# Kernel optimization log

Measured on AMD Instinct MI355X. Metric: run time of the kernel, lower is better.

The kernel has to match this reference:

```python
import jax, jax.numpy as jnp
import numpy as np

NUM_TAGS = 128
BATCH = 128
SEQ = 1024


def setup_inputs() -> dict:
    key = jax.random.key(0)
    k1, k2, k3, k4, k5 = jax.random.split(key, 5)
    emissions = jax.random.normal(k1, (BATCH, SEQ, NUM_TAGS), dtype=jnp.float32)
    tags = jax.random.randint(k2, (BATCH, SEQ), 0, NUM_TAGS, dtype=jnp.int32)
    mask = jnp.ones((BATCH, SEQ), dtype=bool)
    transitions = jax.random.normal(k3, (NUM_TAGS, NUM_TAGS), dtype=jnp.float32)
    start_transitions = jax.random.normal(k4, (NUM_TAGS,), dtype=jnp.float32)
    end_transitions = jax.random.normal(k5, (NUM_TAGS,), dtype=jnp.float32)
    return {
        "emissions": emissions,
        "tags": tags,
        "mask": mask,
        "transitions": transitions,
        "start_transitions": start_transitions,
        "end_transitions": end_transitions,
    }


def _forward_score(emissions, transitions, start_t, end_t, tags, mask):
    # score of the gold path; fully vectorized over time
    first = start_t[tags[:, 0]] + jnp.take_along_axis(emissions[:, 0], tags[:, 0:1], axis=1)[:, 0]
    trans = transitions[tags[:, :-1], tags[:, 1:]]                         # [B, S-1]
    emit = jnp.take_along_axis(emissions[:, 1:], tags[:, 1:, None], axis=2)[..., 0]  # [B, S-1]
    m = mask[:, 1:].astype(emissions.dtype)
    score = first + jnp.sum((trans + emit) * m, axis=1)
    last_idx = jnp.sum(mask, axis=1).astype(jnp.int32) - 1                 # [B]
    last_tags = jnp.take_along_axis(tags, last_idx[:, None], axis=1)[:, 0]
    return score + end_t[last_tags]


def _partition(emissions, transitions, start_t, end_t, mask):
    # log-partition via forward algorithm, single persistent scan over time
    alpha0 = start_t + emissions[:, 0]                                     # [B, T]

    def step(alpha, xs):
        e, mk = xs                                                         # e: [B,T], mk: [B] bool
        # alpha[b,i] + transitions[i,j] + e[b,j]  -> logsumexp over i
        nxt = jax.nn.logsumexp(alpha[:, :, None] + transitions[None, :, :] + e[:, None, :], axis=1)
        return jnp.where(mk[:, None], nxt, alpha), None

    em_t = jnp.swapaxes(emissions[:, 1:], 0, 1)                            # [S-1, B, T]
    mk_t = jnp.swapaxes(mask[:, 1:], 0, 1)                                 # [S-1, B]
    alpha, _ = jax.lax.scan(step, alpha0, (em_t, mk_t))
    return jax.nn.logsumexp(alpha + end_t, axis=1)                         # [B]


def reference(emissions, tags, mask, transitions, start_transitions, end_transitions):
    logZ = _partition(emissions, transitions, start_transitions, end_transitions, mask)
    gold = _forward_score(emissions, transitions, start_transitions, end_transitions, tags, mask)
    return jnp.mean(logZ - gold)
```

## Files before the change

kernel.cpp:

```cpp
#include <hip/hip_runtime.h>

#define NT 128
#define BATCH 128
#define SEQ 1024
#define NSCAN 256

__device__ __forceinline__ float wave_sum64(float x) {
  float y = x;
  asm volatile(
    "v_add_f32 %0, %0, %0 row_shr:1 bound_ctrl:0\n\t"
    "v_add_f32 %0, %0, %0 row_shr:2 bound_ctrl:0\n\t"
    "v_add_f32 %0, %0, %0 row_shr:4 bound_ctrl:0\n\t"
    "v_add_f32 %0, %0, %0 row_shr:8 bound_ctrl:0\n\t"
    "v_add_f32 %0, %0, %0 row_bcast:15 row_mask:0xa\n\t"
    "v_add_f32 %0, %0, %0 row_bcast:31 row_mask:0xc\n\t"
    : "+v"(y));
  return __uint_as_float(__builtin_amdgcn_readlane(__float_as_uint(y), 63));
}

__global__ __attribute__((amdgpu_waves_per_eu(2, 4))) __launch_bounds__(512)
void crf_fused(const float* __restrict__ em, const int* __restrict__ tags,
               const float* __restrict__ trans,
               const float* __restrict__ start_t,
               const float* __restrict__ end_t,
               float* __restrict__ state_out,
               float* __restrict__ shift_out,
               float* __restrict__ gold)
{
  __shared__ float PART[2][4][NT];
  __shared__ float SUMS[2][4];
  __shared__ int   tg[SEQ];
  __shared__ float red[8];

  const int tid = threadIdx.x;
  const int bid = blockIdx.x;

  if (bid < NSCAN) {
    const int l = tid & 63;
    const int w = tid >> 6;
    const int h = w >> 2;
    const int q = w & 3;
    const int b = bid & (BATCH - 1);
    const bool fwd = (bid < BATCH);
    const int jout = h * 64 + l;
    const int isl  = q * 32 + (l & 31);
    const float* emb = em + (size_t)b * SEQ * NT;

    float E[32];
#pragma unroll
    for (int k = 0; k < 32; ++k) {
      float t = fwd ? trans[(q * 32 + k) * NT + jout]
                    : trans[jout * NT + q * 32 + k];
      E[k] = __expf(t);
    }

    const int nsteps = fwd ? 512 : 511;

    float y;
    if (fwd) y = __expf(start_t[isl] + emb[isl]);
    else     y = __expf(end_t[isl] + emb[(size_t)1023 * NT + isl]);

    {
      float ss = wave_sum64(y) * 0.5f;
      if (w < 4 && l == 0) SUMS[0][q] = ss;
    }

    float shift = 0.f;

    float ecur, enx;
    {
      const int r0 = fwd ? 1 : 1022;
      const int r1 = fwd ? 2 : 1021;
      ecur = emb[(size_t)r0 * NT + isl];
      enx  = emb[(size_t)r1 * NT + isl];
    }

    for (int it = 0; it < nsteps; ++it) {
      const int rp = fwd ? (3 + it) : (1020 - it);
      const float pf = emb[(size_t)rp * NT + isl];

      const unsigned yu = __float_as_uint(y);
      float s = 0.f;
#pragma unroll
      for (int k = 0; k < 32; ++k)
        s = fmaf(__uint_as_float(__builtin_amdgcn_readlane(yu, k)), E[k], s);

      const int cb = it & 1;
      PART[cb][q][jout] = s;
      asm volatile("s_waitcnt lgkmcnt(0)" ::: "memory");
      __builtin_amdgcn_s_barrier();
      asm volatile("" ::: "memory");

      float g = (PART[cb][0][isl] + PART[cb][1][isl]) +
                (PART[cb][2][isl] + PART[cb][3][isl]);
      const float4 sv = *(const float4*)&SUMS[cb][0];
      const float uu = (sv.x + sv.y) + (sv.z + sv.w);
      const float rr = __builtin_amdgcn_rcpf(uu);
      shift += __logf(uu);
      const bool apply_em = fwd || (it != nsteps - 1);
      const float ee = apply_em ? __expf(ecur) : 1.0f;
      g = g * rr * ee;
      ecur = enx; enx = pf;

      const float ss = wave_sum64(g) * 0.5f;
      if (w < 4 && l == 0) SUMS[cb ^ 1][q] = ss;
      y = g;
    }

    if (w < 4 && (l & 32) == 0) state_out[bid * NT + isl] = y;
    if (tid == 0) shift_out[bid] = shift;

  } else {
    const int gb = bid - NSCAN;
    const int* tgb = tags + gb * SEQ;
    const float* emb = em + (size_t)gb * SEQ * NT;
    tg[tid] = tgb[tid];
    tg[tid + 512] = tgb[tid + 512];
    __syncthreads();
    float acc = 0.f;
    {
      const int t = tid;
      if (t > 0) acc += trans[tg[t - 1] * NT + tg[t]] + emb[(size_t)t * NT + tg[t]];
      else       acc += start_t[tg[0]] + emb[tg[0]] + end_t[tg[SEQ - 1]];
      const int t2 = tid + 512;
      acc += trans[tg[t2 - 1] * NT + tg[t2]] + emb[(size_t)t2 * NT + tg[t2]];
    }
    const float ws = wave_sum64(acc);
    if ((tid & 63) == 0) red[tid >> 6] = ws;
    __syncthreads();
    if (tid == 0) {
      float r2 = 0.f;
#pragma unroll
      for (int i = 0; i < 8; ++i) r2 += red[i];
      atomicAdd(&gold[gb], r2);
    }
  }
}

__global__ __launch_bounds__(128) void crf_combine(
    const float* __restrict__ state, const float* __restrict__ shift,
    const float* __restrict__ gold, float* __restrict__ out)
{
  const int b = blockIdx.x;
  const int l = threadIdx.x & 63;
  const int w = threadIdx.x >> 6;
  __shared__ float red[2];
  float v = state[b * NT + threadIdx.x] * state[(b + BATCH) * NT + threadIdx.x];
  float ws = wave_sum64(v);
  if (l == 0) red[w] = ws;
  __syncthreads();
  if (threadIdx.x == 0) {
    float logZ = shift[b] + shift[b + BATCH] + __logf(red[0] + red[1]);
    float val = (logZ - gold[b]) * (1.0f / BATCH);
    atomicAdd(out, val);
  }
}

extern "C" void kernel_launch(void* const* d_in, const int* in_sizes, int n_in,
                              void* d_out, int out_size, void* d_ws, size_t ws_size,
                              hipStream_t stream) {
  const float* em    = (const float*)d_in[0];
  const int*   tags  = (const int*)d_in[1];
  const float* trans = (const float*)d_in[3];
  const float* st    = (const float*)d_in[4];
  const float* en    = (const float*)d_in[5];
  float* out = (float*)d_out;

  float* wsf   = (float*)d_ws;
  float* state = wsf;
  float* shift = wsf + 256 * NT;
  float* gold  = shift + 256;

  (void)hipMemsetAsync(d_out, 0, sizeof(float), stream);
  (void)hipMemsetAsync(gold, 0, BATCH * sizeof(float), stream);
  crf_fused<<<NSCAN + BATCH, 512, 0, stream>>>(em, tags, trans, st, en,
                                               state, shift, gold);
  crf_combine<<<BATCH, 128, 0, stream>>>(state, shift, gold, out);
}
```

Baseline: 380.9 us.

## Renormalize CRF forward/backward scan every fourth step and streamline combine

The scan loop now computes the wave sum and rescales alpha only once every four steps instead of every step. It uses a single SUMS buffer, four independent FMA accumulators for the readlane dot product, and pointer-stepped emission prefetch. For the backward direction, the emission at the final step is no longer skipped inside the loop; its factor is divided out after the loop. The gold-score blocks move to the front and write their result directly, so both memsets and the atomics go away, and the combine kernel becomes a single 512-thread block. This shortens the serial per-step dependency chain, at the cost of a larger unnormalized range between rescales and a possible overflow risk.

Result: faster. 308.8 us (-18.9%).

```diff
diff --git a/kernel.cpp b/kernel.cpp
--- a/kernel.cpp
+++ b/kernel.cpp
@@ -3,7 +3,6 @@
 #define NT 128
 #define BATCH 128
 #define SEQ 1024
-#define NSCAN 256
 
 __device__ __forceinline__ float wave_sum64(float x) {
   float y = x;
@@ -18,7 +17,7 @@
   return __uint_as_float(__builtin_amdgcn_readlane(__float_as_uint(y), 63));
 }
 
-__global__ __attribute__((amdgpu_waves_per_eu(2, 4))) __launch_bounds__(512)
+__global__ __attribute__((amdgpu_waves_per_eu(2, 2))) __launch_bounds__(512)
 void crf_fused(const float* __restrict__ em, const int* __restrict__ tags,
                const float* __restrict__ trans,
                const float* __restrict__ start_t,
@@ -28,90 +27,15 @@
                float* __restrict__ gold)
 {
   __shared__ float PART[2][4][NT];
-  __shared__ float SUMS[2][4];
+  __shared__ float SUMS[4];
   __shared__ int   tg[SEQ];
   __shared__ float red[8];
 
   const int tid = threadIdx.x;
   const int bid = blockIdx.x;
 
-  if (bid < NSCAN) {
-    const int l = tid & 63;
-    const int w = tid >> 6;
-    const int h = w >> 2;
-    const int q = w & 3;
-    const int b = bid & (BATCH - 1);
-    const bool fwd = (bid < BATCH);
-    const int jout = h * 64 + l;
-    const int isl  = q * 32 + (l & 31);
-    const float* emb = em + (size_t)b * SEQ * NT;
-
-    float E[32];
-#pragma unroll
-    for (int k = 0; k < 32; ++k) {
-      float t = fwd ? trans[(q * 32 + k) * NT + jout]
-                    : trans[jout * NT + q * 32 + k];
-      E[k] = __expf(t);
-    }
-
-    const int nsteps = fwd ? 512 : 511;
-
-    float y;
-    if (fwd) y = __expf(start_t[isl] + emb[isl]);
-    else     y = __expf(end_t[isl] + emb[(size_t)1023 * NT + isl]);
-
-    {
-      float ss = wave_sum64(y) * 0.5f;
-      if (w < 4 && l == 0) SUMS[0][q] = ss;
-    }
-
-    float shift = 0.f;
-
-    float ecur, enx;
-    {
-      const int r0 = fwd ? 1 : 1022;
-      const int r1 = fwd ? 2 : 1021;
-      ecur = emb[(size_t)r0 * NT + isl];
-      enx  = emb[(size_t)r1 * NT + isl];
-    }
-
-    for (int it = 0; it < nsteps; ++it) {
-      const int rp = fwd ? (3 + it) : (1020 - it);
-      const float pf = emb[(size_t)rp * NT + isl];
-
-      const unsigned yu = __float_as_uint(y);
-      float s = 0.f;
-#pragma unroll
-      for (int k = 0; k < 32; ++k)
-        s = fmaf(__uint_as_float(__builtin_amdgcn_readlane(yu, k)), E[k], s);
-
-      const int cb = it & 1;
-      PART[cb][q][jout] = s;
-      asm volatile("s_waitcnt lgkmcnt(0)" ::: "memory");
-      __builtin_amdgcn_s_barrier();
-      asm volatile("" ::: "memory");
-
-      float g = (PART[cb][0][isl] + PART[cb][1][isl]) +
-                (PART[cb][2][isl] + PART[cb][3][isl]);
-      const float4 sv = *(const float4*)&SUMS[cb][0];
-      const float uu = (sv.x + sv.y) + (sv.z + sv.w);
-      const float rr = __builtin_amdgcn_rcpf(uu);
-      shift += __logf(uu);
-      const bool apply_em = fwd || (it != nsteps - 1);
-      const float ee = apply_em ? __expf(ecur) : 1.0f;
-      g = g * rr * ee;
-      ecur = enx; enx = pf;
-
-      const float ss = wave_sum64(g) * 0.5f;
-      if (w < 4 && l == 0) SUMS[cb ^ 1][q] = ss;
-      y = g;
-    }
-
-    if (w < 4 && (l & 32) == 0) state_out[bid * NT + isl] = y;
-    if (tid == 0) shift_out[bid] = shift;
-
-  } else {
-    const int gb = bid - NSCAN;
+  if (bid < BATCH) {
+    const int gb = bid;
     const int* tgb = tags + gb * SEQ;
     const float* emb = em + (size_t)gb * SEQ * NT;
     tg[tid] = tgb[tid];
@@ -132,27 +56,112 @@
       float r2 = 0.f;
 #pragma unroll
       for (int i = 0; i < 8; ++i) r2 += red[i];
-      atomicAdd(&gold[gb], r2);
+      gold[gb] = r2;
     }
+    return;
   }
+
+  const int sbid = bid - BATCH;
+  const int l = tid & 63;
+  const int w = tid >> 6;
+  const int h = w >> 2;
+  const int q = w & 3;
+  const int b = sbid & (BATCH - 1);
+  const bool fwd = (sbid < BATCH);
+  const int jout = h * 64 + l;
+  const int isl  = q * 32 + (l & 31);
+  const float* emb = em + (size_t)b * SEQ * NT;
+
+  float E[32];
+#pragma unroll
+  for (int k = 0; k < 32; ++k) {
+    float t = fwd ? trans[(q * 32 + k) * NT + jout]
+                  : trans[jout * NT + q * 32 + k];
+    E[k] = __expf(t);
+  }
+
+  const int nsteps = fwd ? 512 : 511;
+
+  float y;
+  if (fwd) y = __expf(start_t[isl] + emb[isl]);
+  else     y = __expf(end_t[isl] + emb[(size_t)1023 * NT + isl]);
+
+  const int dstep = fwd ? NT : -NT;
+  const float* pcur = emb + (fwd ? 1 : 1022) * NT + isl;
+  float ecur = pcur[0];
+  float enx  = pcur[dstep];
+  const float* pp = pcur + 2 * dstep;
+
+  float shift = 0.f;
+
+  for (int it = 0; it < nsteps; ++it) {
+    const float pf = *pp; pp += dstep;
+
+    const unsigned yu = __float_as_uint(y);
+    float s0 = 0.f, s1 = 0.f, s2 = 0.f, s3 = 0.f;
+#pragma unroll
+    for (int k = 0; k < 32; k += 4) {
+      s0 = fmaf(__uint_as_float(__builtin_amdgcn_readlane(yu, k)),     E[k],     s0);
+      s1 = fmaf(__uint_as_float(__builtin_amdgcn_readlane(yu, k + 1)), E[k + 1], s1);
+      s2 = fmaf(__uint_as_float(__builtin_amdgcn_readlane(yu, k + 2)), E[k + 2], s2);
+      s3 = fmaf(__uint_as_float(__builtin_amdgcn_readlane(yu, k + 3)), E[k + 3], s3);
+    }
+    const int cb = it & 1;
+    PART[cb][q][jout] = (s0 + s1) + (s2 + s3);
+
+    asm volatile("s_waitcnt lgkmcnt(0)" ::: "memory");
+    __builtin_amdgcn_s_barrier();
+    asm volatile("" ::: "memory");
+
+    float g = (PART[cb][0][isl] + PART[cb][1][isl]) +
+              (PART[cb][2][isl] + PART[cb][3][isl]);
+    g *= __expf(ecur);
+
+    if ((it & 3) == 3) {
+      const float4 sv = *(const float4*)&SUMS[0];
+      const float uu = (sv.x + sv.y) + (sv.z + sv.w);
+      g *= __builtin_amdgcn_rcpf(uu);
+      shift += __logf(uu);
+    }
+    if ((it & 3) == 2) {
+      const float ss = wave_sum64(g) * 0.5f;
+      if (h == 0 && l == 0) SUMS[q] = ss;
+    }
+
+    ecur = enx; enx = pf;
+    y = g;
+  }
+
+  if (!fwd) y *= __expf(-emb[512 * NT + isl]);
+
+  if (w < 4 && (l & 32) == 0) state_out[sbid * NT + isl] = y;
+  if (tid == 0) shift_out[sbid] = shift;
 }
 
-__global__ __launch_bounds__(128) void crf_combine(
+__global__ __launch_bounds__(512) void crf_combine(
     const float* __restrict__ state, const float* __restrict__ shift,
     const float* __restrict__ gold, float* __restrict__ out)
 {
-  const int b = blockIdx.x;
-  const int l = threadIdx.x & 63;
-  const int w = threadIdx.x >> 6;
-  __shared__ float red[2];
-  float v = state[b * NT + threadIdx.x] * state[(b + BATCH) * NT + threadIdx.x];
-  float ws = wave_sum64(v);
-  if (l == 0) red[w] = ws;
+  const int tid = threadIdx.x;
+  const int b = tid >> 2;
+  const int part = tid & 3;
+  const float* pf = state + b * NT + part * 32;
+  const float* pb = state + (b + BATCH) * NT + part * 32;
+  float s = 0.f;
+#pragma unroll
+  for (int i = 0; i < 32; ++i) s = fmaf(pf[i], pb[i], s);
+  s += __shfl_xor(s, 1);
+  s += __shfl_xor(s, 2);
+  __shared__ float acc[BATCH];
+  if (part == 0) {
+    const float logZ = shift[b] + shift[b + BATCH] + __logf(s);
+    acc[b] = (logZ - gold[b]) * (1.0f / BATCH);
+  }
   __syncthreads();
-  if (threadIdx.x == 0) {
-    float logZ = shift[b] + shift[b + BATCH] + __logf(red[0] + red[1]);
-    float val = (logZ - gold[b]) * (1.0f / BATCH);
-    atomicAdd(out, val);
+  if (tid < 64) {
+    float v = acc[tid] + acc[tid + 64];
+    v = wave_sum64(v);
+    if (tid == 0) out[0] = v;
   }
 }
 
@@ -171,9 +180,7 @@
   float* shift = wsf + 256 * NT;
   float* gold  = shift + 256;
 
-  (void)hipMemsetAsync(d_out, 0, sizeof(float), stream);
-  (void)hipMemsetAsync(gold, 0, BATCH * sizeof(float), stream);
-  crf_fused<<<NSCAN + BATCH, 512, 0, stream>>>(em, tags, trans, st, en,
-                                               state, shift, gold);
-  crf_combine<<<BATCH, 128, 0, stream>>>(state, shift, gold, out);
+  crf_fused<<<3 * BATCH, 512, 0, stream>>>(em, tags, trans, st, en,
+                                           state, shift, gold);
+  crf_combine<<<1, 512, 0, stream>>>(state, shift, gold, out);
 }
```
